# Kernel optimization log

Measured on AMD Instinct MI355X. Metric: run time of the kernel, lower is better.

## Reference

```python
import jax, jax.numpy as jnp
import numpy as np

EMB = 128
B, N = 8, 4096

def setup_inputs() -> dict:
    key = jax.random.key(0)
    k_x, k_q, k_k, k_v = jax.random.split(key, 4)
    return {
        "x": jax.random.normal(k_x, (B, N, EMB), dtype=jnp.float32),
        "w_query": jax.random.uniform(k_q, (EMB, EMB), dtype=jnp.float32),
        "w_key": jax.random.uniform(k_k, (EMB, EMB), dtype=jnp.float32),
        "w_value": jax.random.uniform(k_v, (EMB, EMB), dtype=jnp.float32),
    }

def reference(x, w_query, w_key, w_value):
    # QKV projections: [B, N, D]
    q = jnp.einsum("bnd,de->bne", x, w_query)
    k = jnp.einsum("bnd,de->bne", x, w_key)
    v = jnp.einsum("bnd,de->bne", x, w_value)
    dk = k.shape[-1]
    # scaled dot-product scores: [B, N, N]
    scale = jnp.einsum("bqd,bkd->bqk", q, k) / jnp.sqrt(jnp.float32(dk))
    probs = jax.nn.softmax(scale, axis=2)
    # attention output: [B, N, D]
    return jnp.einsum("bqk,bkd->bqd", probs, v)
```

## Files before the change

### kernel.cpp

```cpp
#include <hip/hip_runtime.h>
#include <hip/hip_bf16.h>

typedef __attribute__((ext_vector_type(4))) float  f32x4;
typedef __attribute__((ext_vector_type(8))) _Float16 h16x8;
typedef __attribute__((ext_vector_type(2))) __fp16 fp16x2;

#define EMB 128
#define NSEQ 4096
#define NB 8
#define SCALE 0.08838834764831845f
#define QSC   (0.08838834764831845f * 1.44269504f)
#define NT    (NSEQ / 64)

__global__ void prep_w(const float* __restrict__ wq, const float* __restrict__ wk,
                       const float* __restrict__ wv, _Float16* __restrict__ whiT,
                       _Float16* __restrict__ wloT) {
    int idx = blockIdx.x * 256 + threadIdx.x;
    if (idx >= 3 * EMB * EMB) return;
    int widx = idx >> 14;
    int rem  = idx & 16383;
    int d = rem >> 7;
    int e = rem & 127;
    const float* w = (widx == 0) ? wq : (widx == 1) ? wk : wv;
    float v = w[d * 128 + e];
    _Float16 hi = (_Float16)v;
    _Float16 lo = (_Float16)(v - (float)hi);
    whiT[(size_t)widx * 16384 + (size_t)e * 128 + d] = hi;
    wloT[(size_t)widx * 16384 + (size_t)e * 128 + d] = lo;
}

__global__ __launch_bounds__(256) void qkv_proj(const float* __restrict__ x,
                                                const _Float16* __restrict__ whiT,
                                                const _Float16* __restrict__ wloT,
                                                _Float16* __restrict__ q,
                                                _Float16* __restrict__ k,
                                                _Float16* __restrict__ vT,
                                                float* __restrict__ aq,
                                                float* __restrict__ ck) {
    const int widx = blockIdx.x >> 9;
    const int blk  = blockIdx.x & 511;
    const int lane = threadIdx.x & 63;
    const int wave = threadIdx.x >> 6;
    const int g    = lane >> 4;
    const int lr   = lane & 15;
    const int rb   = blk * 64 + wave * 16;

    h16x8 xhi[4], xlo[4];
    {
        const float* xrow = x + (size_t)(rb + lr) * EMB;
        #pragma unroll
        for (int kc = 0; kc < 4; ++kc) {
            const float* p = xrow + kc * 32 + g * 8;
            h16x8 ah, al;
            #pragma unroll
            for (int j = 0; j < 8; ++j) {
                float v = p[j];
                _Float16 h = (_Float16)v;
                ah[j] = h;
                al[j] = (_Float16)(v - (float)h);
            }
            xhi[kc] = ah;
            if (widx < 2) xlo[kc] = al;
        }
    }

    const int b  = rb >> 12;
    const int n0 = rb & 4095;

    f32x4 acc[8];
    #pragma unroll
    for (int ct = 0; ct < 8; ++ct) acc[ct] = (f32x4){0.f, 0.f, 0.f, 0.f};

    const _Float16* wh = whiT + (size_t)widx * 16384;
    const _Float16* wl = wloT + (size_t)widx * 16384;
    #pragma unroll
    for (int kc = 0; kc < 4; ++kc) {
        #pragma unroll
        for (int ct = 0; ct < 8; ++ct) {
            size_t off = (size_t)(ct * 16 + lr) * 128 + kc * 32 + g * 8;
            h16x8 bh = *(const h16x8*)(wh + off);
            acc[ct] = __builtin_amdgcn_mfma_f32_16x16x32_f16(xhi[kc], bh, acc[ct], 0, 0, 0);
            if (widx < 2) {
                h16x8 bl = *(const h16x8*)(wl + off);
                acc[ct] = __builtin_amdgcn_mfma_f32_16x16x32_f16(xlo[kc], bh, acc[ct], 0, 0, 0);
                acc[ct] = __builtin_amdgcn_mfma_f32_16x16x32_f16(xhi[kc], bl, acc[ct], 0, 0, 0);
            }
        }
    }

    if (widx < 2) {
        float c[4];
        #pragma unroll
        for (int r = 0; r < 4; ++r) {
            float rs = 0.f;
            #pragma unroll
            for (int ct = 0; ct < 8; ++ct) rs += acc[ct][r];
            #pragma unroll
            for (int off = 8; off; off >>= 1) rs += __shfl_xor(rs, off);
            c[r] = rs * (1.0f / 128.0f);
        }
        if (widx == 0) {
            #pragma unroll
            for (int ct = 0; ct < 8; ++ct)
                #pragma unroll
                for (int r = 0; r < 4; ++r) {
                    size_t row = rb + g * 4 + r;
                    q[row * 128 + ct * 16 + lr] = (_Float16)((acc[ct][r] - c[r]) * QSC);
                }
            if (lr == 0) {
                #pragma unroll
                for (int r = 0; r < 4; ++r) aq[rb + g * 4 + r] = c[r] * 128.0f * QSC;
            }
        } else {
            #pragma unroll
            for (int ct = 0; ct < 8; ++ct)
                #pragma unroll
                for (int r = 0; r < 4; ++r) {
                    size_t row = rb + g * 4 + r;
                    k[row * 128 + ct * 16 + lr] = (_Float16)(acc[ct][r] - c[r]);
                }
            if (lr == 0) {
                #pragma unroll
                for (int r = 0; r < 4; ++r) ck[rb + g * 4 + r] = c[r];
            }
        }
    } else {
        #pragma unroll
        for (int ct = 0; ct < 8; ++ct)
            #pragma unroll
            for (int r = 0; r < 4; ++r) {
                int e  = ct * 16 + lr;
                int nn = n0 + g * 4 + r;
                vT[((size_t)b * EMB + e) * NSEQ + nn] = (_Float16)acc[ct][r];
            }
    }
}

__global__ __launch_bounds__(256, 2) void flash(const _Float16* __restrict__ q,
                                                const _Float16* __restrict__ k,
                                                const _Float16* __restrict__ vT,
                                                const float* __restrict__ aq,
                                                const float* __restrict__ ck,
                                                float* __restrict__ O0,
                                                float* __restrict__ O1,
                                                float* __restrict__ m0a, float* __restrict__ l0a,
                                                float* __restrict__ m1a, float* __restrict__ l1a) {
    __shared__ __align__(16) char KsB[2][16384];
    __shared__ __align__(16) char VsB[2][16384];

    const int bp  = blockIdx.x;
    const int bid = (bp & 7) * 64 + (bp >> 3);

    const int lane = threadIdx.x & 63;
    const int wave = threadIdx.x >> 6;
    const int g    = lane >> 4;
    const int lr   = lane & 15;
    const int b    = bid >> 6;
    const int rem  = bid & 63;
    const int qt   = rem & 31;
    const int half = rem >> 5;
    const int t0   = half * (NT / 2);
    const size_t baseA = (size_t)b * NSEQ + qt * 128 + wave * 32;
    const size_t baseB = baseA + 16;

    float* __restrict__ Opart = half ? O1 : O0;
    float* __restrict__ mArr  = half ? m1a : m0a;
    float* __restrict__ lArr  = half ? l1a : l0a;

    const _Float16* kbat = k  + (size_t)b * NSEQ * EMB;
    const _Float16* vbat = vT + (size_t)b * EMB * NSEQ;
    const float*    ckb  = ck + (size_t)b * NSEQ;

    h16x8 qfA[4], qfB[4];
    #pragma unroll
    for (int kc = 0; kc < 4; ++kc) {
        qfA[kc] = *(const h16x8*)(q + (baseA + lr) * 128 + kc * 32 + g * 8);
        qfB[kc] = *(const h16x8*)(q + (baseB + lr) * 128 + kc * 32 + g * 8);
    }
    const float aqvA = aq[baseA + lr];
    const float aqvB = aq[baseB + lr];

    const int r64   = threadIdx.x >> 2;
    const int kcolB = (threadIdx.x & 3) * 64;
    const int kslot = ((r64 >> 5) * 2 + ((r64 >> 2) & 1)) * 16 + (((r64 >> 3) & 3) << 2) + (r64 & 3);
    const char* kp = (const char*)(kbat + (size_t)(t0 * 64 + r64) * EMB) + kcolB;
    const int kdst = kslot * 256;
    const int kswz = (kslot & 15) << 4;

    const int vrow  = threadIdx.x >> 1;
    const int vcolB = (threadIdx.x & 1) * 64;
    const char* vp = (const char*)(vbat + (size_t)vrow * NSEQ) + vcolB + (size_t)t0 * 128;
    const int vdst = vrow * 128;
    const int vswz = (vrow & 7) << 4;

    h16x8 stK[4], stV[4];
    #pragma unroll
    for (int i = 0; i < 4; ++i) stK[i] = *(const h16x8*)(kp + i * 16);
    #pragma unroll
    for (int i = 0; i < 4; ++i) stV[i] = *(const h16x8*)(vp + i * 16);
    #pragma unroll
    for (int i = 0; i < 4; ++i)
        *(h16x8*)(KsB[0] + kdst + ((kcolB + i * 16) ^ kswz)) = stK[i];
    #pragma unroll
    for (int i = 0; i < 4; ++i)
        *(h16x8*)(VsB[0] + vdst + ((vcolB + i * 16) ^ vswz)) = stV[i];
    __syncthreads();

    f32x4 oA[8], oB[8];
    #pragma unroll
    for (int ct = 0; ct < 8; ++ct) {
        oA[ct] = (f32x4){0.f, 0.f, 0.f, 0.f};
        oB[ct] = (f32x4){0.f, 0.f, 0.f, 0.f};
    }
    float mA = -1e30f, mB = -1e30f;
    float lA = 0.f, lB = 0.f;

    int cur = 0;
    for (int t = t0; t < t0 + NT / 2; ++t) {
        kp += 16384; vp += 128;
        if (t + 1 < t0 + NT / 2) {
            #pragma unroll
            for (int i = 0; i < 4; ++i) stK[i] = *(const h16x8*)(kp + i * 16);
            #pragma unroll
            for (int i = 0; i < 4; ++i) stV[i] = *(const h16x8*)(vp + i * 16);
        }

        f32x4 ckt[4];
        #pragma unroll
        for (int ct = 0; ct < 4; ++ct)
            ckt[ct] = *(const f32x4*)(ckb + t * 64 + (ct >> 1) * 32 + (ct & 1) * 4 + g * 8);

        const char* Kb = KsB[cur];
        f32x4 sA[4], sB[4];
        __builtin_amdgcn_s_setprio(1);
        #pragma unroll
        for (int ct = 0; ct < 4; ++ct) {
            f32x4 aA = (f32x4){0.f, 0.f, 0.f, 0.f};
            f32x4 aB = (f32x4){0.f, 0.f, 0.f, 0.f};
            #pragma unroll
            for (int kc = 0; kc < 4; ++kc) {
                h16x8 kb = *(const h16x8*)(Kb + (ct * 16 + lr) * 256 + ((kc * 64 + g * 16) ^ (lr << 4)));
                aA = __builtin_amdgcn_mfma_f32_16x16x32_f16(kb, qfA[kc], aA, 0, 0, 0);
                aB = __builtin_amdgcn_mfma_f32_16x16x32_f16(kb, qfB[kc], aB, 0, 0, 0);
            }
            #pragma unroll
            for (int r = 0; r < 4; ++r) {
                aA[r] += aqvA * ckt[ct][r];
                aB[r] += aqvB * ckt[ct][r];
            }
            sA[ct] = aA;
            sB[ct] = aB;
        }
        __builtin_amdgcn_s_setprio(0);

        float tmA = sA[0][0], tmB = sB[0][0];
        #pragma unroll
        for (int ct = 0; ct < 4; ++ct)
            #pragma unroll
            for (int r = 0; r < 4; ++r) {
                tmA = fmaxf(tmA, sA[ct][r]);
                tmB = fmaxf(tmB, sB[ct][r]);
            }
        tmA = fmaxf(tmA, __shfl_xor(tmA, 16));
        tmA = fmaxf(tmA, __shfl_xor(tmA, 32));
        tmB = fmaxf(tmB, __shfl_xor(tmB, 16));
        tmB = fmaxf(tmB, __shfl_xor(tmB, 32));
        if (__any((tmA > mA + 11.544f) || (tmB > mB + 11.544f))) {
            float mnA = fmaxf(mA, tmA), mnB = fmaxf(mB, tmB);
            float scA = exp2f(mA - mnA), scB = exp2f(mB - mnB);
            mA = mnA; mB = mnB;
            lA *= scA; lB *= scB;
            float osA[4], osB[4];
            #pragma unroll
            for (int r = 0; r < 4; ++r) {
                osA[r] = __shfl(scA, (lane & 48) | (g * 4 + r));
                osB[r] = __shfl(scB, (lane & 48) | (g * 4 + r));
            }
            #pragma unroll
            for (int ct = 0; ct < 8; ++ct)
                #pragma unroll
                for (int r = 0; r < 4; ++r) {
                    oA[ct][r] *= osA[r];
                    oB[ct][r] *= osB[r];
                }
        }
        #pragma unroll
        for (int ct = 0; ct < 4; ++ct)
            #pragma unroll
            for (int r = 0; r < 4; ++r) {
                float pA = exp2f(sA[ct][r] - mA);
                float pB = exp2f(sB[ct][r] - mB);
                sA[ct][r] = pA; sB[ct][r] = pB;
                lA += pA; lB += pB;
            }

        h16x8 paA[2], paB[2];
        #pragma unroll
        for (int w = 0; w < 2; ++w) {
            fp16x2 a01 = __builtin_amdgcn_cvt_pkrtz(sA[2 * w][0], sA[2 * w][1]);
            fp16x2 a23 = __builtin_amdgcn_cvt_pkrtz(sA[2 * w][2], sA[2 * w][3]);
            fp16x2 a45 = __builtin_amdgcn_cvt_pkrtz(sA[2 * w + 1][0], sA[2 * w + 1][1]);
            fp16x2 a67 = __builtin_amdgcn_cvt_pkrtz(sA[2 * w + 1][2], sA[2 * w + 1][3]);
            fp16x2 b01 = __builtin_amdgcn_cvt_pkrtz(sB[2 * w][0], sB[2 * w][1]);
            fp16x2 b23 = __builtin_amdgcn_cvt_pkrtz(sB[2 * w][2], sB[2 * w][3]);
            fp16x2 b45 = __builtin_amdgcn_cvt_pkrtz(sB[2 * w + 1][0], sB[2 * w + 1][1]);
            fp16x2 b67 = __builtin_amdgcn_cvt_pkrtz(sB[2 * w + 1][2], sB[2 * w + 1][3]);
            h16x8 a8, b8;
            a8[0] = (_Float16)a01[0]; a8[1] = (_Float16)a01[1];
            a8[2] = (_Float16)a23[0]; a8[3] = (_Float16)a23[1];
            a8[4] = (_Float16)a45[0]; a8[5] = (_Float16)a45[1];
            a8[6] = (_Float16)a67[0]; a8[7] = (_Float16)a67[1];
            b8[0] = (_Float16)b01[0]; b8[1] = (_Float16)b01[1];
            b8[2] = (_Float16)b23[0]; b8[3] = (_Float16)b23[1];
            b8[4] = (_Float16)b45[0]; b8[5] = (_Float16)b45[1];
            b8[6] = (_Float16)b67[0]; b8[7] = (_Float16)b67[1];
            paA[w] = a8;
            paB[w] = b8;
        }

        const char* Vb = VsB[cur];
        __builtin_amdgcn_s_setprio(1);
        #pragma unroll
        for (int ct = 0; ct < 8; ++ct) {
            #pragma unroll
            for (int w = 0; w < 2; ++w) {
                h16x8 vb = *(const h16x8*)(Vb + (ct * 16 + lr) * 128 + ((w * 64 + g * 16) ^ ((lr & 7) << 4)));
                oA[ct] = __builtin_amdgcn_mfma_f32_16x16x32_f16(paA[w], vb, oA[ct], 0, 0, 0);
                oB[ct] = __builtin_amdgcn_mfma_f32_16x16x32_f16(paB[w], vb, oB[ct], 0, 0, 0);
            }
        }
        __builtin_amdgcn_s_setprio(0);

        if (t + 1 < t0 + NT / 2) {
            char* kw = (char*)KsB[cur ^ 1];
            char* vw = (char*)VsB[cur ^ 1];
            #pragma unroll
            for (int i = 0; i < 4; ++i)
                *(h16x8*)(kw + kdst + ((kcolB + i * 16) ^ kswz)) = stK[i];
            #pragma unroll
            for (int i = 0; i < 4; ++i)
                *(h16x8*)(vw + vdst + ((vcolB + i * 16) ^ vswz)) = stV[i];
        }
        __syncthreads();
        cur ^= 1;
    }

    lA += __shfl_xor(lA, 16);
    lA += __shfl_xor(lA, 32);
    lB += __shfl_xor(lB, 16);
    lB += __shfl_xor(lB, 32);
    if (lane < 16) {
        mArr[baseA + lr] = mA;  lArr[baseA + lr] = lA;
        mArr[baseB + lr] = mB;  lArr[baseB + lr] = lB;
    }
    #pragma unroll
    for (int ct = 0; ct < 8; ++ct)
        #pragma unroll
        for (int r = 0; r < 4; ++r) {
            size_t rowA = baseA + g * 4 + r;
            size_t rowB = baseB + g * 4 + r;
            Opart[rowA * EMB + ct * 16 + lr] = oA[ct][r];
            Opart[rowB * EMB + ct * 16 + lr] = oB[ct][r];
        }
}

__global__ __launch_bounds__(256) void merge_halves(const float* __restrict__ O1,
                                                    const float* __restrict__ m0a,
                                                    const float* __restrict__ l0a,
                                                    const float* __restrict__ m1a,
                                                    const float* __restrict__ l1a,
                                                    float* __restrict__ out) {
    int gid = blockIdx.x * 256 + threadIdx.x;
    int row = gid >> 4;
    int c0  = (gid & 15) * 8;
    float mm0 = m0a[row], mm1 = m1a[row];
    float M   = fmaxf(mm0, mm1);
    float w0  = exp2f(mm0 - M), w1 = exp2f(mm1 - M);
    float inv = 1.0f / (l0a[row] * w0 + l1a[row] * w1);
    float*       p0 = out + (size_t)row * EMB + c0;
    const float* p1 = O1  + (size_t)row * EMB + c0;
    f32x4 a0 = *(const f32x4*)p0, a1 = *(const f32x4*)(p0 + 4);
    f32x4 b0 = *(const f32x4*)p1, b1 = *(const f32x4*)(p1 + 4);
    f32x4 r0 = (a0 * w0 + b0 * w1) * inv;
    f32x4 r1 = (a1 * w0 + b1 * w1) * inv;
    *(f32x4*)p0       = r0;
    *(f32x4*)(p0 + 4) = r1;
}

extern "C" void kernel_launch(void* const* d_in, const int* in_sizes, int n_in,
                              void* d_out, int out_size, void* d_ws, size_t ws_size,
                              hipStream_t stream) {
    const float* x  = (const float*)d_in[0];
    const float* wq = (const float*)d_in[1];
    const float* wk = (const float*)d_in[2];
    const float* wv = (const float*)d_in[3];

    char* ws = (char*)d_ws;
    _Float16* q    = (_Float16*)(ws);
    _Float16* kk   = (_Float16*)(ws + 8388608);
    _Float16* vT   = (_Float16*)(ws + 16777216);
    float*    aq   = (float*)   (ws + 25165824);
    float*    ck   = (float*)   (ws + 25296896);
    _Float16* whiT = (_Float16*)(ws + 25427968);
    _Float16* wloT = (_Float16*)(ws + 25526272);
    float*    O1   = (float*)   (ws + 25690112);
    float*    m0a  = (float*)   (ws + 42467328);
    float*    l0a  = (float*)   (ws + 42598400);
    float*    m1a  = (float*)   (ws + 42729472);
    float*    l1a  = (float*)   (ws + 42860544);

    prep_w<<<192, 256, 0, stream>>>(wq, wk, wv, whiT, wloT);
    qkv_proj<<<1536, 256, 0, stream>>>(x, whiT, wloT, q, kk, vT, aq, ck);
    flash<<<512, 256, 0, stream>>>(q, kk, vT, aq, ck,
                                   (float*)d_out, O1, m0a, l0a, m1a, l1a);
    merge_halves<<<2048, 256, 0, stream>>>(O1, m0a, l0a, m1a, l1a, (float*)d_out);
}
```

Measured before the change: 163.5 us.

## Store K/V as pre-swizzled LDS tile images and stage via direct global-to-LDS loads

The projection kernel now writes K and V straight into per-tile byte images that already carry the swizzled shared-memory layout the flash kernel expects. The flash kernel then copies each 16KB tile into LDS with global_load_lds instructions instead of loading into registers and storing to LDS by hand. This removes the staging registers and the LDS write instructions from the inner loop, which lowers register pressure and VALU/LDS issue. In exchange, the projection kernel does scattered 2-byte stores. The last loop iteration also issues a redundant reload into the idle buffer, and it is unclear whether the asynchronous load completion is properly waited on before the barrier.

```diff
diff --git a/kernel.cpp b/kernel.cpp
--- a/kernel.cpp
+++ b/kernel.cpp
@@ -4,6 +4,8 @@
 typedef __attribute__((ext_vector_type(4))) float  f32x4;
 typedef __attribute__((ext_vector_type(8))) _Float16 h16x8;
 typedef __attribute__((ext_vector_type(2))) __fp16 fp16x2;
+typedef const __attribute__((address_space(1))) unsigned int guint;
+typedef __attribute__((address_space(3))) unsigned int luint;
 
 #define EMB 128
 #define NSEQ 4096
@@ -33,8 +35,8 @@
                                                 const _Float16* __restrict__ whiT,
                                                 const _Float16* __restrict__ wloT,
                                                 _Float16* __restrict__ q,
-                                                _Float16* __restrict__ k,
-                                                _Float16* __restrict__ vT,
+                                                char* __restrict__ kimg,
+                                                char* __restrict__ vimg,
                                                 float* __restrict__ aq,
                                                 float* __restrict__ ck) {
     const int widx = blockIdx.x >> 9;
@@ -116,8 +118,14 @@
             for (int ct = 0; ct < 8; ++ct)
                 #pragma unroll
                 for (int r = 0; r < 4; ++r) {
-                    size_t row = rb + g * 4 + r;
-                    k[row * 128 + ct * 16 + lr] = (_Float16)(acc[ct][r] - c[r]);
+                    int nn  = n0 + g * 4 + r;
+                    int tt  = nn >> 6, r64 = nn & 63;
+                    int slot = ((r64 >> 5) * 2 + ((r64 >> 2) & 1)) * 16
+                             + (((r64 >> 3) & 3) << 2) + (r64 & 3);
+                    int e = ct * 16 + lr;
+                    size_t byte = ((size_t)(b * 64 + tt) << 14) + slot * 256
+                                + ((2 * e) ^ ((slot & 15) << 4));
+                    *(_Float16*)(kimg + byte) = (_Float16)(acc[ct][r] - c[r]);
                 }
             if (lr == 0) {
                 #pragma unroll
@@ -131,14 +139,17 @@
             for (int r = 0; r < 4; ++r) {
                 int e  = ct * 16 + lr;
                 int nn = n0 + g * 4 + r;
-                vT[((size_t)b * EMB + e) * NSEQ + nn] = (_Float16)acc[ct][r];
+                int tt = nn >> 6, kv = nn & 63;
+                size_t byte = ((size_t)(b * 64 + tt) << 14) + e * 128
+                            + ((2 * kv) ^ ((e & 7) << 4));
+                *(_Float16*)(vimg + byte) = (_Float16)acc[ct][r];
             }
     }
 }
 
 __global__ __launch_bounds__(256, 2) void flash(const _Float16* __restrict__ q,
-                                                const _Float16* __restrict__ k,
-                                                const _Float16* __restrict__ vT,
+                                                const char* __restrict__ kimg,
+                                                const char* __restrict__ vimg,
                                                 const float* __restrict__ aq,
                                                 const float* __restrict__ ck,
                                                 float* __restrict__ O0,
@@ -167,9 +178,9 @@
     float* __restrict__ mArr  = half ? m1a : m0a;
     float* __restrict__ lArr  = half ? l1a : l0a;
 
-    const _Float16* kbat = k  + (size_t)b * NSEQ * EMB;
-    const _Float16* vbat = vT + (size_t)b * EMB * NSEQ;
-    const float*    ckb  = ck + (size_t)b * NSEQ;
+    const char* kimg_b = kimg + ((size_t)b << 20);
+    const char* vimg_b = vimg + ((size_t)b << 20);
+    const float* ckb   = ck + (size_t)b * NSEQ;
 
     h16x8 qfA[4], qfB[4];
     #pragma unroll
@@ -180,30 +191,19 @@
     const float aqvA = aq[baseA + lr];
     const float aqvB = aq[baseB + lr];
 
-    const int r64   = threadIdx.x >> 2;
-    const int kcolB = (threadIdx.x & 3) * 64;
-    const int kslot = ((r64 >> 5) * 2 + ((r64 >> 2) & 1)) * 16 + (((r64 >> 3) & 3) << 2) + (r64 & 3);
-    const char* kp = (const char*)(kbat + (size_t)(t0 * 64 + r64) * EMB) + kcolB;
-    const int kdst = kslot * 256;
-    const int kswz = (kslot & 15) << 4;
-
-    const int vrow  = threadIdx.x >> 1;
-    const int vcolB = (threadIdx.x & 1) * 64;
-    const char* vp = (const char*)(vbat + (size_t)vrow * NSEQ) + vcolB + (size_t)t0 * 128;
-    const int vdst = vrow * 128;
-    const int vswz = (vrow & 7) << 4;
-
-    h16x8 stK[4], stV[4];
-    #pragma unroll
-    for (int i = 0; i < 4; ++i) stK[i] = *(const h16x8*)(kp + i * 16);
-    #pragma unroll
-    for (int i = 0; i < 4; ++i) stV[i] = *(const h16x8*)(vp + i * 16);
-    #pragma unroll
-    for (int i = 0; i < 4; ++i)
-        *(h16x8*)(KsB[0] + kdst + ((kcolB + i * 16) ^ kswz)) = stK[i];
-    #pragma unroll
-    for (int i = 0; i < 4; ++i)
-        *(h16x8*)(VsB[0] + vdst + ((vcolB + i * 16) ^ vswz)) = stV[i];
+    auto stage = [&](int tile, int buf) {
+        const char* ks = kimg_b + ((size_t)tile << 14) + wave * 4096 + lane * 16;
+        const char* vs = vimg_b + ((size_t)tile << 14) + wave * 4096 + lane * 16;
+        char* kd = (char*)KsB[buf] + wave * 4096;
+        char* vd = (char*)VsB[buf] + wave * 4096;
+        #pragma unroll
+        for (int i = 0; i < 4; ++i) {
+            __builtin_amdgcn_global_load_lds((guint*)(ks + i * 1024), (luint*)(kd + i * 1024), 16, 0, 0);
+            __builtin_amdgcn_global_load_lds((guint*)(vs + i * 1024), (luint*)(vd + i * 1024), 16, 0, 0);
+        }
+    };
+
+    stage(t0, 0);
     __syncthreads();
 
     f32x4 oA[8], oB[8];
@@ -217,13 +217,8 @@
 
     int cur = 0;
     for (int t = t0; t < t0 + NT / 2; ++t) {
-        kp += 16384; vp += 128;
-        if (t + 1 < t0 + NT / 2) {
-            #pragma unroll
-            for (int i = 0; i < 4; ++i) stK[i] = *(const h16x8*)(kp + i * 16);
-            #pragma unroll
-            for (int i = 0; i < 4; ++i) stV[i] = *(const h16x8*)(vp + i * 16);
-        }
+        int tn = (t + 1 < t0 + NT / 2) ? t + 1 : t;
+        stage(tn, cur ^ 1);
 
         f32x4 ckt[4];
         #pragma unroll
@@ -331,16 +326,6 @@
         }
         __builtin_amdgcn_s_setprio(0);
 
-        if (t + 1 < t0 + NT / 2) {
-            char* kw = (char*)KsB[cur ^ 1];
-            char* vw = (char*)VsB[cur ^ 1];
-            #pragma unroll
-            for (int i = 0; i < 4; ++i)
-                *(h16x8*)(kw + kdst + ((kcolB + i * 16) ^ kswz)) = stK[i];
-            #pragma unroll
-            for (int i = 0; i < 4; ++i)
-                *(h16x8*)(vw + vdst + ((vcolB + i * 16) ^ vswz)) = stV[i];
-        }
         __syncthreads();
         cur ^= 1;
     }
@@ -397,8 +382,8 @@
 
     char* ws = (char*)d_ws;
     _Float16* q    = (_Float16*)(ws);
-    _Float16* kk   = (_Float16*)(ws + 8388608);
-    _Float16* vT   = (_Float16*)(ws + 16777216);
+    char*     kimg = (char*)    (ws + 8388608);
+    char*     vimg = (char*)    (ws + 16777216);
     float*    aq   = (float*)   (ws + 25165824);
     float*    ck   = (float*)   (ws + 25296896);
     _Float16* whiT = (_Float16*)(ws + 25427968);
@@ -410,8 +395,8 @@
     float*    l1a  = (float*)   (ws + 42860544);
 
     prep_w<<<192, 256, 0, stream>>>(wq, wk, wv, whiT, wloT);
-    qkv_proj<<<1536, 256, 0, stream>>>(x, whiT, wloT, q, kk, vT, aq, ck);
-    flash<<<512, 256, 0, stream>>>(q, kk, vT, aq, ck,
+    qkv_proj<<<1536, 256, 0, stream>>>(x, whiT, wloT, q, kimg, vimg, aq, ck);
+    flash<<<512, 256, 0, stream>>>(q, kimg, vimg, aq, ck,
                                    (float*)d_out, O1, m0a, l0a, m1a, l1a);
     merge_halves<<<2048, 256, 0, stream>>>(O1, m0a, l0a, m1a, l1a, (float*)d_out);
 }
```

After: 159.2 us. 2.6% less time.
